# Performance work log

Hardware: AMD Instinct MI355X
Metric: run time of the kernel (lower is better)

The kernel has to match this reference:

```python
import jax, jax.numpy as jnp
import numpy as np

N = 10000        # nodes
E = 160000       # edges (avg degree 16)
MUL = 128        # channel multiplicity
A = 10           # node-attr (species one-hot) dim
RAD = 8          # radial bessel features
INV_SQRT3 = 0.5773502691896258  # CG coefficient for 1o x 1o -> 0e


def _mlp(x, Ws):
    # RadialMLP: linear layers with SiLU between, no activation on last
    for W in Ws[:-1]:
        x = jax.nn.silu(x @ W)
    return x @ Ws[-1]


def setup_inputs() -> dict:
    key = jax.random.key(0)
    ks = jax.random.split(key, 25)

    def g(k, shape):
        return jax.random.normal(k, shape, jnp.float32) / np.float32(np.sqrt(shape[0]))

    return {
        "node_attrs": jax.random.uniform(ks[0], (N, A), jnp.float32),
        "node_feats": jax.random.normal(ks[1], (N, 4 * MUL), jnp.float32),
        "edge_attrs": jax.random.normal(ks[2], (E, 4), jnp.float32),
        "edge_feats": jax.random.uniform(ks[3], (E, RAD), jnp.float32),
        "W_src": g(ks[5], (A, MUL)),
        "W_tgt": g(ks[6], (A, MUL)),
        "W_up0": g(ks[7], (MUL, MUL)),
        "W_up1": g(ks[8], (MUL, MUL)),
        "W_skip0": g(ks[9], (MUL, MUL)),
        "W_skip1": g(ks[10], (MUL, MUL)),
        "W_res0": g(ks[11], (MUL, 2 * MUL)),
        "W_res1": g(ks[12], (MUL, MUL)),
        "W_lin1_0": g(ks[13], (2 * MUL, 2 * MUL)),
        "W_lin1_1": g(ks[14], (2 * MUL, MUL)),
        "W_lin2_0": g(ks[15], (MUL, MUL)),
        "W_lin2_1": g(ks[16], (MUL, MUL)),
        "W_rad1": g(ks[17], (RAD + 2 * MUL, 64)),
        "W_rad2": g(ks[18], (64, 64)),
        "W_rad3": g(ks[19], (64, 64)),
        "W_rad4": g(ks[20], (64, 4 * MUL)),
        "W_den1": g(ks[21], (RAD + 2 * MUL, 64)),
        "W_den2": g(ks[22], (64, 1)),
        "alpha": jnp.ones((), jnp.float32),   # scaled by 20 inside (alpha = param * 20)
        "beta": jnp.zeros((), jnp.float32),
        "edge_index": jax.random.randint(ks[4], (E, 2), 0, N),
    }


def _forward(node_attrs, node_feats, edge_attrs, edge_feats,
             W_src, W_tgt, W_up0, W_up1, W_skip0, W_skip1, W_res0, W_res1,
             W_lin1_0, W_lin1_1, W_lin2_0, W_lin2_1,
             W_rad1, W_rad2, W_rad3, W_rad4, W_den1, W_den2,
             alpha, beta, edge_index):
    n = node_feats.shape[0]
    # split node feats into 128x0e scalars and 128x1o vectors (mul_ir layout)
    s = node_feats[:, :MUL]                           # [N, 128]
    v = node_feats[:, MUL:].reshape(n, MUL, 3)        # [N, 128, 3]

    # skip connection: Linear(node_feats_irreps -> hidden_irreps)
    sc_s = s @ W_skip0
    sc_v = jnp.einsum("nui,uv->nvi", v, W_skip1)
    sc = jnp.concatenate([sc_s, sc_v.reshape(n, -1)], axis=-1)  # [N, 512]

    # linear_up (node_feats -> edge_irreps) and linear_res (-> irreps_nonlin)
    up_s = s @ W_up0
    up_v = jnp.einsum("nui,uv->nvi", v, W_up1)
    res_s = s @ W_res0                                # [N, 256] (scalars + gates)
    res_v = jnp.einsum("nui,uv->nvi", v, W_res1)      # [N, 128, 3]

    # per-species scalar embeddings, gathered per edge
    src_emb = node_attrs @ W_src                      # [N, 128]
    tgt_emb = node_attrs @ W_tgt
    snd = edge_index[:, 0]
    rcv = edge_index[:, 1]
    aug = jnp.concatenate([edge_feats, src_emb[snd], tgt_emb[rcv]], axis=-1)  # [E, 264]

    # radial MLP -> per-edge tensor-product weights; density MLP
    tpw = _mlp(aug, [W_rad1, W_rad2, W_rad3, W_rad4])  # [E, 512]
    edge_density = jnp.tanh(_mlp(aug, [W_den1, W_den2]) ** 2)  # [E, 1]
    density = jax.ops.segment_sum(edge_density, rcv, num_segments=n)  # [N, 1]

    # equivariant tensor product (uvu, per-edge weights), lmax=1 CG paths
    xs = up_s[snd]                                    # [E, 128]
    xv = up_v[snd]                                    # [E, 128, 3]
    y0 = edge_attrs[:, :1]                            # [E, 1]
    y1 = edge_attrs[:, 1:4]                           # [E, 3]
    wA, wB, wC, wD = jnp.split(tpw, 4, axis=-1)
    mA = wA * xs * y0                                               # 0e x 0e -> 0e
    mD = wD * jnp.einsum("eui,ei->eu", xv, y1) * INV_SQRT3          # 1o x 1o -> 0e
    mB = (wB * xs)[:, :, None] * y1[:, None, :]                     # 0e x 1o -> 1o
    mC = wC[:, :, None] * xv * y0[:, :, None]                       # 1o x 0e -> 1o
    m_s = jnp.concatenate([mA, mD], axis=-1)          # [E, 256]
    m_v = jnp.concatenate([mB, mC], axis=1)           # [E, 256, 3]

    # scatter-add messages to receiver nodes
    msg_s = jax.ops.segment_sum(m_s, rcv, num_segments=n)  # [N, 256]
    msg_v = jax.ops.segment_sum(m_v, rcv, num_segments=n)  # [N, 256, 3]

    # linear_1 (irreps_mid -> irreps_nonlin), density normalization, residual
    msg_s = msg_s @ W_lin1_0                          # [N, 256]
    msg_v = jnp.einsum("nui,uv->nvi", msg_v, W_lin1_1)  # [N, 128, 3]
    denom = density * beta + alpha * 20.0             # [N, 1]
    msg_s = msg_s / denom + res_s
    msg_v = msg_v / denom[..., None] + res_v

    # equivariant gate nonlinearity: silu on scalars, sigmoid gates on vectors
    scal = jax.nn.silu(msg_s[:, :MUL])
    gate = jax.nn.sigmoid(msg_s[:, MUL:])
    vec = msg_v * gate[:, :, None]

    # linear_2 and reshape to [N, channels, (lmax+1)^2]
    out_s = scal @ W_lin2_0                           # [N, 128]
    out_v = jnp.einsum("nui,uv->nvi", vec, W_lin2_1)  # [N, 128, 3]
    message = jnp.concatenate([out_s[:, :, None], out_v], axis=-1)  # [N, 128, 4]
    return message, sc


def reference(node_attrs, node_feats, edge_attrs, edge_feats,
              W_src, W_tgt, W_up0, W_up1, W_skip0, W_skip1, W_res0, W_res1,
              W_lin1_0, W_lin1_1, W_lin2_0, W_lin2_1,
              W_rad1, W_rad2, W_rad3, W_rad4, W_den1, W_den2,
              alpha, beta, edge_index):
    return _forward(node_attrs, node_feats, edge_attrs, edge_feats,
                    W_src, W_tgt, W_up0, W_up1, W_skip0, W_skip1, W_res0, W_res1,
                    W_lin1_0, W_lin1_1, W_lin2_0, W_lin2_1,
                    W_rad1, W_rad2, W_rad3, W_rad4, W_den1, W_den2,
                    alpha, beta, edge_index)
```

## Files before the change

kernel.cpp:

```cpp
#include <hip/hip_runtime.h>
#include <hip/hip_bf16.h>
#include <math.h>

#define NN 10000
#define NE 160000
#define MUL 128
#define ADIM 10
#define RADF 8
#define HID 64
#define INV_SQRT3 0.57735026918962576f
#define NB64 157

typedef __attribute__((ext_vector_type(8))) short bf16x8;
typedef __attribute__((ext_vector_type(4))) float f32x4;

__device__ __forceinline__ float silu_f(float x){ return x / (1.0f + __expf(-x)); }
__device__ __forceinline__ float sigmoid_f(float x){ return 1.0f / (1.0f + __expf(-x)); }
__device__ __forceinline__ unsigned short f2b(float f){
  union{float f; unsigned u;} v; v.f=f;
  unsigned r = (v.u + 0x7fffu + ((v.u>>16)&1u))>>16;
  return (unsigned short)r;
}
__device__ __forceinline__ unsigned short f2bh(float f){
  __hip_bfloat16 h = __float2bfloat16(f);
  union{ __hip_bfloat16 h; unsigned short u; } v; v.h=h; return v.u;
}
__device__ __forceinline__ unsigned f2b2(float lo, float hi){
  float2 t; t.x=lo; t.y=hi;
  __hip_bfloat162 h2 = __float22bfloat162_rn(t);
  union{ __hip_bfloat162 h; unsigned u; } v; v.h=h2; return v.u;
}
__device__ __forceinline__ float b2f(unsigned short h){
  union{unsigned u; float f;} v; v.u = ((unsigned)h)<<16; return v.f;
}
__device__ __forceinline__ float b2f_lo(unsigned u){
  union{unsigned u; float f;} v; v.u = u<<16; return v.f;
}
__device__ __forceinline__ float b2f_hi(unsigned u){
  union{unsigned u; float f;} v; v.u = u & 0xffff0000u; return v.f;
}

__global__ __launch_bounds__(256) void k_nodeemb(
    const float* __restrict__ attrs, const float* __restrict__ Wc,
    float* __restrict__ pA, float* __restrict__ pB){
  int idx = blockIdx.x*256 + threadIdx.x;
  if (idx >= NN*64) return;
  int n = idx>>6, c = idx&63;
  float s0=0,s1=0,s2=0,s3=0;
  #pragma unroll
  for (int a=0;a<ADIM;a++){
    float x = attrs[n*ADIM+a];
    s0 += x*Wc[(0*ADIM+a)*64+c];
    s1 += x*Wc[(1*ADIM+a)*64+c];
    s2 += x*Wc[(2*ADIM+a)*64+c];
    s3 += x*Wc[(3*ADIM+a)*64+c];
  }
  pA[(size_t)n*128 + c*2 + 0] = s0;
  pA[(size_t)n*128 + c*2 + 1] = s2;
  pB[(size_t)n*128 + c*2 + 0] = s1;
  pB[(size_t)n*128 + c*2 + 1] = s3;
}

__global__ __launch_bounds__(256) void k_feat_prep(
    const float* __restrict__ feats, unsigned short* __restrict__ fs16,
    unsigned short* __restrict__ fv16){
  int idx = blockIdx.x*256 + threadIdx.x;
  int n = idx >> 9, c = idx & 511;
  float v = feats[idx];
  if (c < 128) fs16[n*128 + c] = f2bh(v);
  else {
    int q = c - 128; int u = q/3; int i = q - 3*u;
    fv16[((size_t)n*3 + i)*128 + u] = f2bh(v);
  }
}

__global__ __launch_bounds__(256) void k_prep(
    const float* __restrict__ Wr2, const float* __restrict__ Wr3,
    const float* __restrict__ Wr4,
    const float* __restrict__ Wl10, const float* __restrict__ Wl11,
    const float* __restrict__ Wl20, const float* __restrict__ Wl21,
    const float* __restrict__ Wsk0, const float* __restrict__ Wup0, const float* __restrict__ Wres0,
    const float* __restrict__ Wsk1, const float* __restrict__ Wup1, const float* __restrict__ Wres1,
    const float* __restrict__ Wsrc, const float* __restrict__ Wtgt,
    const float* __restrict__ Wr1, const float* __restrict__ Wd1,
    unsigned short* __restrict__ WTr2, unsigned short* __restrict__ WTr3,
    unsigned short* __restrict__ WTr4,
    unsigned short* __restrict__ Wl10T, unsigned short* __restrict__ Wl11T,
    unsigned short* __restrict__ Wl20T, unsigned short* __restrict__ Wl21T,
    unsigned short* __restrict__ WnsT, unsigned short* __restrict__ WnvT,
    float* __restrict__ Wc){
  int idx = blockIdx.x*256 + threadIdx.x;
  if (idx < 4096){
    int j = idx; int n=j>>6, k=j&63;
    WTr2[j] = f2b(Wr2[k*64+n]);
  } else if (idx < 8192){
    int j = idx-4096; int n=j>>6, k=j&63;
    WTr3[j] = f2b(Wr3[k*64+n]);
  } else if (idx < 40960){
    int j = idx-8192; int n=j>>6, k=j&63;
    WTr4[j] = f2b(Wr4[k*512+n]);
  } else if (idx < 106496){
    int j = idx-40960; int n=j>>8, k=j&255;
    Wl10T[j] = f2b(Wl10[k*256+n]);
  } else if (idx < 139264){
    int j = idx-106496; int n=j>>8, k=j&255;
    Wl11T[j] = f2b(Wl11[k*128+n]);
  } else if (idx < 155648){
    int j = idx-139264; int n=j>>7, k=j&127;
    Wl20T[j] = f2b(Wl20[k*128+n]);
  } else if (idx < 172032){
    int j = idx-155648; int n=j>>7, k=j&127;
    Wl21T[j] = f2b(Wl21[k*128+n]);
  } else if (idx < 237568){
    int j = idx-172032; int n=j>>7, k=j&127;
    float v;
    if (n < 128)      v = Wsk0[k*128+n];
    else if (n < 256) v = Wup0[k*128+(n-128)];
    else              v = Wres0[k*256+(n-256)];
    WnsT[j] = f2b(v);
  } else if (idx < 286720){
    int j = idx-237568; int n=j>>7, k=j&127;
    float v;
    if (n < 128)      v = Wsk1[k*128+n];
    else if (n < 256) v = Wup1[k*128+(n-128)];
    else              v = Wres1[k*128+(n-256)];
    WnvT[j] = f2b(v);
  } else if (idx < 286976){
    int j = idx - 286720;
    int m = j>>6, c = j&63;
    const float* WA = (m&1)? Wtgt : Wsrc;
    const float* WB = (m<2)? Wr1 : Wd1;
    int koff = (m&1)? 136 : 8;
    for (int a=0;a<ADIM;a++){
      float s=0.f;
      for (int k=0;k<128;k++) s += WA[a*128+k]*WB[(koff+k)*64+c];
      Wc[(m*ADIM+a)*64+c] = s;
    }
  }
}

__global__ __launch_bounds__(256) void k_node_pre2(
    const unsigned short* __restrict__ fs16, const unsigned short* __restrict__ fv16,
    const unsigned short* __restrict__ WnsT, const unsigned short* __restrict__ WnvT,
    float* __restrict__ out_sc,
    unsigned short* __restrict__ upk16,
    float* __restrict__ res_s, float* __restrict__ res_v){
  __shared__ unsigned short fA[64][136];
  int nb = blockIdx.x*64;
  int c = blockIdx.y;
  int g, ntc;
  if (c < 4){ g=0; ntc=c; } else { g = 1 + (c-4)/3; ntc = (c-4)%3; }
  int tid = threadIdx.x;
  int w = tid>>6, l = tid&63, m0 = w*16, lr = l&15, lg = l>>4;
  for (int idx=tid; idx<64*16; idx+=256){
    int row = idx>>4, s8 = idx&15;
    int n = min(nb+row, NN-1);
    const unsigned short* src = (g==0) ? &fs16[(size_t)n*128 + s8*8]
                                       : &fv16[((size_t)n*3 + (g-1))*128 + s8*8];
    *(uint4*)&fA[row][s8*8] = *(const uint4*)src;
  }
  __syncthreads();
  const unsigned short* WT = ((g==0)? WnsT : WnvT) + (size_t)ntc*128*128;
  f32x4 acc[8];
  #pragma unroll
  for (int t=0;t<8;t++) acc[t]=(f32x4)(0.f);
  #pragma unroll
  for (int kb=0;kb<4;kb++){
    bf16x8 a = *(const bf16x8*)&fA[m0+lr][kb*32 + lg*8];
    #pragma unroll
    for (int t=0;t<8;t++){
      bf16x8 b = *(const bf16x8*)&WT[(size_t)(t*16+lr)*128 + kb*32 + lg*8];
      acc[t] = __builtin_amdgcn_mfma_f32_16x16x32_bf16(a, b, acc[t], 0,0,0);
    }
  }
  #pragma unroll
  for (int t=0;t<8;t++){
    #pragma unroll
    for (int r=0;r<4;r++){
      int col = (ntc*8+t)*16 + lr;
      int row = m0 + lg*4 + r;
      int n = nb + row;
      if (n < NN){
        float v = acc[t][r];
        if (g==0){
          if (col < 128)      out_sc[(size_t)n*512 + col] = v;
          else if (col < 256){
            int cc = col-128;
            upk16[(size_t)n*512 + (cc&63)*8 + (cc>>6)] = f2bh(v);
          } else              res_s[(size_t)n*256 + col-256] = v;
        } else {
          int i = g-1;
          if (col < 128)      out_sc[(size_t)n*512 + 128 + col*3 + i] = v;
          else if (col < 256){
            int cc = col-128;
            upk16[(size_t)n*512 + (cc&63)*8 + (1+i)*2 + (cc>>6)] = f2bh(v);
          } else              res_v[((size_t)n*3+i)*128 + col-256] = v;
        }
      }
    }
  }
}

__global__ __launch_bounds__(256) void k_deg(const int* __restrict__ eidx, int* __restrict__ deg){
  int i = blockIdx.x*256+threadIdx.x;
  if (i<NE) atomicAdd(&deg[eidx[2*i+1]],1);
}
__global__ __launch_bounds__(256) void k_scan(const int* __restrict__ deg, int* __restrict__ offsets){
  __shared__ int part[256];
  int t = threadIdx.x; int base = t*40;
  int s=0;
  for (int k=0;k<40;k++){ int idx=base+k; if (idx<NN) s+=deg[idx]; }
  part[t]=s; __syncthreads();
  if (t==0){ int run=0; for (int i=0;i<256;i++){ int v=part[i]; part[i]=run; run+=v; } }
  __syncthreads();
  int run = part[t];
  for (int k=0;k<40;k++){
    int idx=base+k;
    if (idx<=NN) offsets[idx]=run;
    if (idx<NN) run+=deg[idx];
  }
}
__global__ __launch_bounds__(256) void k_fill(
    const int* __restrict__ eidx, const float* __restrict__ ef, const float* __restrict__ ea,
    const int* __restrict__ offsets, int* __restrict__ cursor,
    int* __restrict__ sndbuf, int* __restrict__ rcvbuf,
    float4* __restrict__ ybuf, float* __restrict__ efb){
  int i = blockIdx.x*256+threadIdx.x;
  if (i<NE){
    int sn = eidx[2*i], rc = eidx[2*i+1];
    int p = offsets[rc] + atomicAdd(&cursor[rc],1);
    sndbuf[p]=sn; rcvbuf[p]=rc;
    ybuf[p] = ((const float4*)ea)[i];
    *(float4*)&efb[(size_t)p*8]     = *(const float4*)&ef[(size_t)i*8];
    *(float4*)&efb[(size_t)p*8 + 4] = *(const float4*)&ef[(size_t)i*8 + 4];
  }
}

__global__ __launch_bounds__(256) void k_tpw(
    const int* __restrict__ sndbuf, const int* __restrict__ rcvbuf,
    const float* __restrict__ efb,
    const float* __restrict__ pA, const float* __restrict__ pB,
    const float* __restrict__ Wr1, const float* __restrict__ Wd1, const float* __restrict__ Wd2,
    const unsigned short* __restrict__ WTr2, const unsigned short* __restrict__ WTr3,
    const unsigned short* __restrict__ WTr4,
    const int* __restrict__ offsets, int nstart, int nend, int cap,
    unsigned* __restrict__ tpwp, float* __restrict__ densbuf){
  __shared__ unsigned short hA[64][72];
  __shared__ unsigned short hB[64][72];
  int ebase = offsets[nstart];
  int eend  = min(offsets[nend], ebase + cap);
  int i0 = ebase + blockIdx.x*64;
  if (i0 >= eend) return;
  int nrows = min(64, eend - i0);
  int tid = threadIdx.x;
  int w = tid>>6, l = tid&63, m0 = w*16, lr = l&15, lg = l>>4;
  int wbase = i0 + m0;
  int v_meta = 0;
  {
    int pos = min(wbase + (l&15), eend-1);
    if (l < 16)      v_meta = sndbuf[pos];
    else if (l < 32) v_meta = rcvbuf[pos];
  }
  float ra, rb;
  {
    int pos = min(wbase + (l&15), eend-1);
    ra = efb[(size_t)pos*8 + (l>>4)];
    rb = efb[(size_t)pos*8 + 4 + (l>>4)];
  }
  {
    float wr[8], wd[8];
    #pragma unroll
    for (int k=0;k<8;k++){ wr[k]=Wr1[k*64+l]; wd[k]=Wd1[k*64+l]; }
    float wd2c = Wd2[l];
    #pragma unroll
    for (int j=0;j<16;j++){
      int sn = __shfl(v_meta, j);
      int rc = __shfl(v_meta, 16+j);
      float2 av = *(const float2*)&pA[(size_t)sn*128 + l*2];
      float2 bv = *(const float2*)&pB[(size_t)rc*128 + l*2];
      float e0=__shfl(ra,j),    e1=__shfl(ra,16+j), e2=__shfl(ra,32+j), e3=__shfl(ra,48+j);
      float e4=__shfl(rb,j),    e5=__shfl(rb,16+j), e6=__shfl(rb,32+j), e7=__shfl(rb,48+j);
      float h  = av.x + bv.x;
      float hd = av.y + bv.y;
      h  += e0*wr[0]+e1*wr[1]+e2*wr[2]+e3*wr[3]+e4*wr[4]+e5*wr[5]+e6*wr[6]+e7*wr[7];
      hd += e0*wd[0]+e1*wd[1]+e2*wd[2]+e3*wd[3]+e4*wd[4]+e5*wd[5]+e6*wd[6]+e7*wd[7];
      hA[m0+j][l] = f2bh(silu_f(h));
      float sv = silu_f(hd)*wd2c;
      #pragma unroll
      for (int m=32;m;m>>=1) sv += __shfl_xor(sv, m);
      if (l==0 && m0+j < nrows) densbuf[wbase + j] = tanhf(sv*sv);
    }
  }
  f32x4 acc[4];
  #pragma unroll
  for (int nt=0;nt<4;nt++) acc[nt]=(f32x4)(0.f);
  #pragma unroll
  for (int kb=0;kb<2;kb++){
    bf16x8 a = *(const bf16x8*)&hA[m0+lr][kb*32 + lg*8];
    #pragma unroll
    for (int nt=0;nt<4;nt++){
      bf16x8 b = *(const bf16x8*)&WTr2[(nt*16+lr)*64 + kb*32 + lg*8];
      acc[nt] = __builtin_amdgcn_mfma_f32_16x16x32_bf16(a, b, acc[nt], 0,0,0);
    }
  }
  #pragma unroll
  for (int nt=0;nt<4;nt++)
    #pragma unroll
    for (int r=0;r<4;r++)
      hB[m0+lg*4+r][nt*16+lr] = f2bh(silu_f(acc[nt][r]));
  #pragma unroll
  for (int nt=0;nt<4;nt++) acc[nt]=(f32x4)(0.f);
  #pragma unroll
  for (int kb=0;kb<2;kb++){
    bf16x8 a = *(const bf16x8*)&hB[m0+lr][kb*32 + lg*8];
    #pragma unroll
    for (int nt=0;nt<4;nt++){
      bf16x8 b = *(const bf16x8*)&WTr3[(nt*16+lr)*64 + kb*32 + lg*8];
      acc[nt] = __builtin_amdgcn_mfma_f32_16x16x32_bf16(a, b, acc[nt], 0,0,0);
    }
  }
  #pragma unroll
  for (int nt=0;nt<4;nt++)
    #pragma unroll
    for (int r=0;r<4;r++)
      hA[m0+lg*4+r][nt*16+lr] = f2bh(silu_f(acc[nt][r]));
  int erow0 = i0 - ebase;
  #pragma unroll
  for (int nt=0; nt<4; nt++){
    unsigned pvv[4][4];
    #pragma unroll
    for (int G=0; G<4; G++){
      f32x4 aE=(f32x4)(0.f), aO=(f32x4)(0.f);
      #pragma unroll
      for (int kb=0; kb<2; kb++){
        bf16x8 a  = *(const bf16x8*)&hA[m0+lr][kb*32 + lg*8];
        bf16x8 bE = *(const bf16x8*)&WTr4[((2*G)*64+nt*16+lr)*64 + kb*32 + lg*8];
        bf16x8 bO = *(const bf16x8*)&WTr4[((2*G+1)*64+nt*16+lr)*64 + kb*32 + lg*8];
        aE = __builtin_amdgcn_mfma_f32_16x16x32_bf16(a, bE, aE, 0,0,0);
        aO = __builtin_amdgcn_mfma_f32_16x16x32_bf16(a, bO, aO, 0,0,0);
      }
      #pragma unroll
      for (int r=0;r<4;r++)
        pvv[r][G] = f2b2(aE[r], aO[r]);
    }
    #pragma unroll
    for (int r=0;r<4;r++){
      int row = m0 + lg*4 + r;
      if (row < nrows)
        *(uint4*)&tpwp[(size_t)(erow0+row)*256 + (nt*16+lr)*4] = *(uint4*)&pvv[r][0];
    }
  }
}

__global__ __launch_bounds__(256) void k_gather(
    const unsigned* __restrict__ tpwp, const float4* __restrict__ ybuf,
    const int* __restrict__ sndbuf, const float* __restrict__ densbuf,
    const uint4* __restrict__ upk4,
    const int* __restrict__ offsets, int nstart,
    unsigned short* __restrict__ msg_s16, unsigned short* __restrict__ msg_v16,
    float* __restrict__ density){
  __shared__ float part[2][1024];
  __shared__ float pden[2];
  int w = threadIdx.x>>6, l = threadIdx.x&63;
  int pairIdx = w>>1, half = w&1;
  int n = nstart + blockIdx.x*2 + pairIdx;
  int ebase = offsets[nstart];
  int s0 = offsets[n], s1 = offsets[n+1];
  float mA0=0,mA1=0,mD0=0,mD1=0;
  float mB00=0,mB01=0,mB10=0,mB11=0,mB20=0,mB21=0;
  float mC00=0,mC01=0,mC10=0,mC11=0,mC20=0,mC21=0;
  float dsum=0;
  for (int i=s0+half; i<s1; i+=2){
    int li = i - ebase;
    int sn = sndbuf[i];
    float4 y = ybuf[i];
    dsum += densbuf[i];
    uint4 tq = *(const uint4*)&tpwp[(size_t)li*256 + l*4];
    uint4 uq = upk4[(size_t)sn*64 + l];
    float wA0=b2f_lo(tq.x), wA1=b2f_hi(tq.x);
    float wB0=b2f_lo(tq.y), wB1=b2f_hi(tq.y);
    float wC0=b2f_lo(tq.z), wC1=b2f_hi(tq.z);
    float wD0=b2f_lo(tq.w), wD1=b2f_hi(tq.w);
    float xs0=b2f_lo(uq.x), xs1=b2f_hi(uq.x);
    float xv00=b2f_lo(uq.y), xv01=b2f_hi(uq.y);
    float xv10=b2f_lo(uq.z), xv11=b2f_hi(uq.z);
    float xv20=b2f_lo(uq.w), xv21=b2f_hi(uq.w);
    mA0 += wA0*xs0*y.x; mA1 += wA1*xs1*y.x;
    float dot0 = xv00*y.y + xv10*y.z + xv20*y.w;
    float dot1 = xv01*y.y + xv11*y.z + xv21*y.w;
    mD0 += wD0*dot0; mD1 += wD1*dot1;
    float b0 = wB0*xs0, b1 = wB1*xs1;
    mB00 += b0*y.y; mB01 += b1*y.y;
    mB10 += b0*y.z; mB11 += b1*y.z;
    mB20 += b0*y.w; mB21 += b1*y.w;
    float c0 = wC0*y.x, c1 = wC1*y.x;
    mC00 += c0*xv00; mC01 += c1*xv01;
    mC10 += c0*xv10; mC11 += c1*xv11;
    mC20 += c0*xv20; mC21 += c1*xv21;
  }
  if (half==1){
    float* P = part[pairIdx];
    P[0*64+l]=mA0;  P[1*64+l]=mA1;  P[2*64+l]=mD0;  P[3*64+l]=mD1;
    P[4*64+l]=mB00; P[5*64+l]=mB01; P[6*64+l]=mB10; P[7*64+l]=mB11;
    P[8*64+l]=mB20; P[9*64+l]=mB21; P[10*64+l]=mC00; P[11*64+l]=mC01;
    P[12*64+l]=mC10; P[13*64+l]=mC11; P[14*64+l]=mC20; P[15*64+l]=mC21;
    if (l==0) pden[pairIdx]=dsum;
  }
  __syncthreads();
  if (half==0){
    const float* P = part[pairIdx];
    mA0+=P[0*64+l];  mA1+=P[1*64+l];  mD0+=P[2*64+l];  mD1+=P[3*64+l];
    mB00+=P[4*64+l]; mB01+=P[5*64+l]; mB10+=P[6*64+l]; mB11+=P[7*64+l];
    mB20+=P[8*64+l]; mB21+=P[9*64+l]; mC00+=P[10*64+l]; mC01+=P[11*64+l];
    mC10+=P[12*64+l]; mC11+=P[13*64+l]; mC20+=P[14*64+l]; mC21+=P[15*64+l];
    dsum += pden[pairIdx];
    unsigned short* ms = msg_s16 + (size_t)n*256;
    ms[l]=f2bh(mA0); ms[64+l]=f2bh(mA1);
    ms[128+l]=f2bh(mD0*INV_SQRT3); ms[192+l]=f2bh(mD1*INV_SQRT3);
    unsigned short* mv = msg_v16 + (size_t)n*768;
    mv[l]=f2bh(mB00);     mv[64+l]=f2bh(mB01);  mv[128+l]=f2bh(mC00); mv[192+l]=f2bh(mC01);
    mv[256+l]=f2bh(mB10); mv[320+l]=f2bh(mB11); mv[384+l]=f2bh(mC10); mv[448+l]=f2bh(mC11);
    mv[512+l]=f2bh(mB20); mv[576+l]=f2bh(mB21); mv[640+l]=f2bh(mC20); mv[704+l]=f2bh(mC21);
    if (l==0) density[n]=dsum;
  }
}

__global__ __launch_bounds__(256) void k_post1(
    const unsigned short* __restrict__ msg_s16, const unsigned short* __restrict__ msg_v16,
    const float* __restrict__ density,
    const float* __restrict__ res_s, const float* __restrict__ res_v,
    const unsigned short* __restrict__ Wl10T, const unsigned short* __restrict__ Wl11T,
    const float* __restrict__ alphap, const float* __restrict__ betap,
    unsigned short* __restrict__ scal16, unsigned short* __restrict__ gate16,
    unsigned short* __restrict__ vtmp16){
  __shared__ unsigned short sm[64][264];
  __shared__ float sden[64];
  int nb = blockIdx.x*64, y = blockIdx.y;
  int tid = threadIdx.x;
  int w = tid>>6, l = tid&63, m0 = w*16, lr = l&15, lg = l>>4;
  for (int idx=tid; idx<64*32; idx+=256){
    int row = idx>>5, s8 = idx&31;
    int n = min(nb+row, NN-1);
    const unsigned short* src = (y<2)? &msg_s16[(size_t)n*256 + s8*8]
                                     : &msg_v16[(size_t)n*768 + (y-2)*256 + s8*8];
    *(uint4*)&sm[row][s8*8] = *(const uint4*)src;
  }
  if (tid < 64){
    int n = min(nb+tid, NN-1);
    sden[tid] = density[n]*betap[0] + alphap[0]*20.0f;
  }
  __syncthreads();
  const unsigned short* BT = (y<2)? (Wl10T + (size_t)y*128*256) : Wl11T;
  f32x4 acc[8];
  #pragma unroll
  for (int t=0;t<8;t++) acc[t]=(f32x4)(0.f);
  for (int kb=0;kb<8;kb++){
    bf16x8 a = *(const bf16x8*)&sm[m0+lr][kb*32 + lg*8];
    #pragma unroll
    for (int t=0;t<8;t++){
      bf16x8 b = *(const bf16x8*)&BT[(size_t)(t*16+lr)*256 + kb*32 + lg*8];
      acc[t] = __builtin_amdgcn_mfma_f32_16x16x32_bf16(a, b, acc[t], 0,0,0);
    }
  }
  #pragma unroll
  for (int t=0;t<8;t++){
    #pragma unroll
    for (int r=0;r<4;r++){
      int col = t*16+lr;
      int row = m0 + lg*4 + r;
      int n = nb + row;
      if (n < NN){
        float v = acc[t][r]/sden[row];
        if (y==0){
          v += res_s[(size_t)n*256 + col];
          scal16[(size_t)n*128 + col] = f2bh(silu_f(v));
        } else if (y==1){
          v += res_s[(size_t)n*256 + 128 + col];
          gate16[(size_t)n*128 + col] = f2bh(sigmoid_f(v));
        } else {
          int i = y-2;
          v += res_v[((size_t)n*3+i)*128 + col];
          vtmp16[((size_t)i*NN + n)*128 + col] = f2bh(v);
        }
      }
    }
  }
}

__global__ __launch_bounds__(256) void k_post2(
    const unsigned short* __restrict__ scal16, const unsigned short* __restrict__ gate16,
    const unsigned short* __restrict__ vtmp16,
    const unsigned short* __restrict__ Wl20T, const unsigned short* __restrict__ Wl21T,
    float* __restrict__ out_msg){
  __shared__ unsigned short sA[64][136];
  int nb = blockIdx.x*64, y = blockIdx.y;
  int tid = threadIdx.x;
  int w = tid>>6, l = tid&63, m0 = w*16, lr = l&15, lg = l>>4;
  for (int idx=tid; idx<64*16; idx+=256){
    int row = idx>>4, s8 = idx&15;
    int n = min(nb+row, NN-1);
    if (y==0){
      *(uint4*)&sA[row][s8*8] = *(const uint4*)&scal16[(size_t)n*128 + s8*8];
    } else {
      int i = y-1;
      uint4 va = *(const uint4*)&vtmp16[((size_t)i*NN + n)*128 + s8*8];
      uint4 vg = *(const uint4*)&gate16[(size_t)n*128 + s8*8];
      const unsigned short* pa = (const unsigned short*)&va;
      const unsigned short* pg = (const unsigned short*)&vg;
      unsigned short o[8];
      #pragma unroll
      for (int j=0;j<8;j++) o[j] = f2bh(b2f(pa[j])*b2f(pg[j]));
      *(uint4*)&sA[row][s8*8] = *(const uint4*)o;
    }
  }
  __syncthreads();
  const unsigned short* BT = (y==0)? Wl20T : Wl21T;
  f32x4 acc[8];
  #pragma unroll
  for (int t=0;t<8;t++) acc[t]=(f32x4)(0.f);
  #pragma unroll
  for (int kb=0;kb<4;kb++){
    bf16x8 a = *(const bf16x8*)&sA[m0+lr][kb*32 + lg*8];
    #pragma unroll
    for (int t=0;t<8;t++){
      bf16x8 b = *(const bf16x8*)&BT[(size_t)(t*16+lr)*128 + kb*32 + lg*8];
      acc[t] = __builtin_amdgcn_mfma_f32_16x16x32_bf16(a, b, acc[t], 0,0,0);
    }
  }
  #pragma unroll
  for (int t=0;t<8;t++){
    #pragma unroll
    for (int r=0;r<4;r++){
      int col = t*16+lr;
      int n = nb + m0 + lg*4 + r;
      if (n < NN) out_msg[(size_t)n*512 + col*4 + y] = acc[t][r];
    }
  }
}

extern "C" void kernel_launch(void* const* d_in, const int* in_sizes, int n_in,
                              void* d_out, int out_size, void* d_ws, size_t ws_size,
                              hipStream_t stream){
  (void)in_sizes; (void)n_in; (void)out_size;
  const float* attrs = (const float*)d_in[0];
  const float* feats = (const float*)d_in[1];
  const float* ea    = (const float*)d_in[2];
  const float* ef    = (const float*)d_in[3];
  const float* Wsrc  = (const float*)d_in[4];
  const float* Wtgt  = (const float*)d_in[5];
  const float* Wup0  = (const float*)d_in[6];
  const float* Wup1  = (const float*)d_in[7];
  const float* Wsk0  = (const float*)d_in[8];
  const float* Wsk1  = (const float*)d_in[9];
  const float* Wres0 = (const float*)d_in[10];
  const float* Wres1 = (const float*)d_in[11];
  const float* Wl10  = (const float*)d_in[12];
  const float* Wl11  = (const float*)d_in[13];
  const float* Wl20  = (const float*)d_in[14];
  const float* Wl21  = (const float*)d_in[15];
  const float* Wr1   = (const float*)d_in[16];
  const float* Wr2   = (const float*)d_in[17];
  const float* Wr3   = (const float*)d_in[18];
  const float* Wr4   = (const float*)d_in[19];
  const float* Wd1   = (const float*)d_in[20];
  const float* Wd2   = (const float*)d_in[21];
  const float* alphap= (const float*)d_in[22];
  const float* betap = (const float*)d_in[23];
  const int*   eidx  = (const int*)d_in[24];

  const size_t fixed_bytes =
      (size_t)NN*(512 + 1536 + 1024 + 1536 + 4 + 1024 + 256 + 768 + 512 + 512 + 256) +
      (size_t)NE*60 +
      (size_t)286976*2 + 4*ADIM*64*4 +
      (10240+10240+10256)*4 + 64*256;
  int nchunk, npc, cap;
  if (fixed_bytes + (size_t)NE*1024 + 65536 <= ws_size){ nchunk=1; npc=NN;   cap=NE;    }
  else if (fixed_bytes + 81920ULL*1024 + 65536 <= ws_size){ nchunk=2; npc=5000; cap=81920; }
  else { nchunk=4; npc=2500; cap=44032; }

  char* p = (char*)d_ws;
  auto alloc = [&](size_t bytes)->char*{ char* r=p; p += (bytes+255)&~(size_t)255; return r; };
  unsigned* tpwp  = (unsigned*)alloc((size_t)cap*256*4);
  unsigned short* msg_s16 = (unsigned short*)alloc((size_t)NN*256*2);
  unsigned short* msg_v16 = (unsigned short*)alloc((size_t)NN*768*2);
  float*  res_s   = (float*)alloc((size_t)NN*256*4);
  float*  res_v   = (float*)alloc((size_t)NN*384*4);
  float*  density = (float*)alloc((size_t)NN*4);
  float4* ybuf    = (float4*)alloc((size_t)NE*16);
  float*  densbuf = (float*)alloc((size_t)NE*4);
  int*    sndbuf  = (int*)alloc((size_t)NE*4);
  int*    rcvbuf  = (int*)alloc((size_t)NE*4);
  float*  efb     = (float*)alloc((size_t)NE*32);
  uint4*  upk     = (uint4*)alloc((size_t)NN*64*16);
  unsigned short* fs16 = (unsigned short*)alloc((size_t)NN*128*2);
  unsigned short* fv16 = (unsigned short*)alloc((size_t)NN*384*2);
  float* pA = (float*)alloc((size_t)NN*128*4);
  float* pB = (float*)alloc((size_t)NN*128*4);
  float* Wc  = (float*)alloc(4*ADIM*64*4);
  unsigned short* gate16 = (unsigned short*)alloc((size_t)NN*128*2);
  unsigned short* WTr2 = (unsigned short*)alloc(4096*2);
  unsigned short* WTr3 = (unsigned short*)alloc(4096*2);
  unsigned short* WTr4 = (unsigned short*)alloc(32768*2);
  unsigned short* Wl10T = (unsigned short*)alloc(65536*2);
  unsigned short* Wl11T = (unsigned short*)alloc(32768*2);
  unsigned short* Wl20T = (unsigned short*)alloc(16384*2);
  unsigned short* Wl21T = (unsigned short*)alloc(16384*2);
  unsigned short* WnsT  = (unsigned short*)alloc(65536*2);
  unsigned short* WnvT  = (unsigned short*)alloc(49152*2);
  int* deg     = (int*)alloc(10240*4);
  int* cursor  = (int*)alloc(10240*4);
  int* offsets = (int*)alloc(10256*4);

  unsigned short* scal16 = fs16;
  unsigned short* vtmp16 = fv16;

  float* out_msg = (float*)d_out;
  float* out_sc  = out_msg + (size_t)NN*512;

  hipMemsetAsync(deg, 0, 2*10240*sizeof(int), stream);

  k_prep<<<1121, 256, 0, stream>>>(Wr2, Wr3, Wr4, Wl10, Wl11, Wl20, Wl21,
                                   Wsk0, Wup0, Wres0, Wsk1, Wup1, Wres1,
                                   Wsrc, Wtgt, Wr1, Wd1,
                                   WTr2, WTr3, WTr4,
                                   Wl10T, Wl11T, Wl20T, Wl21T, WnsT, WnvT, Wc);
  k_nodeemb<<<(NN*64+255)/256, 256, 0, stream>>>(attrs, Wc, pA, pB);
  k_feat_prep<<<NN*512/256, 256, 0, stream>>>(feats, fs16, fv16);
  k_node_pre2<<<dim3(NB64,13), 256, 0, stream>>>(fs16, fv16, WnsT, WnvT,
                                                 out_sc, (unsigned short*)upk, res_s, res_v);
  k_deg<<<(NE+255)/256, 256, 0, stream>>>(eidx, deg);
  k_scan<<<1, 256, 0, stream>>>(deg, offsets);
  k_fill<<<(NE+255)/256, 256, 0, stream>>>(eidx, ef, ea, offsets, cursor,
                                           sndbuf, rcvbuf, ybuf, efb);

  int tpw_blocks = (cap+63)/64;
  for (int c=0; c<nchunk; ++c){
    k_tpw<<<tpw_blocks, 256, 0, stream>>>(sndbuf, rcvbuf, efb, pA, pB,
                                          Wr1, Wd1, Wd2, WTr2, WTr3, WTr4,
                                          offsets, c*npc, (c+1)*npc, cap,
                                          tpwp, densbuf);
    k_gather<<<npc/2, 256, 0, stream>>>(tpwp, ybuf, sndbuf, densbuf, upk,
                                        offsets, c*npc, msg_s16, msg_v16, density);
  }

  k_post1<<<dim3(NB64,5), 256, 0, stream>>>(msg_s16, msg_v16, density, res_s, res_v,
                                            Wl10T, Wl11T, alphap, betap,
                                            scal16, gate16, vtmp16);
  k_post2<<<dim3(NB64,4), 256, 0, stream>>>(scal16, gate16, vtmp16,
                                            Wl20T, Wl21T, out_msg);
}
```

Before: 442.9 us.

## Fuse edge MLP with receiver segmented reduction, add boundary fixup kernel

Merges the per-edge radial MLP kernel and the per-node gather kernel into one. Each wave takes a fixed 16-edge window, reduces it by receiver segment in registers, and writes interior segments straight to fp32 message buffers. Segments that cross a window boundary go to head/tail partial buffers, which a new fixup kernel combines. This removes the large bf16 per-edge weight buffer, its write and re-read, and the chunk loop. The cost is extra fp32 message traffic, a memset of the message buffers, and scattered boundary writes.

```diff
diff --git a/kernel.cpp b/kernel.cpp
--- a/kernel.cpp
+++ b/kernel.cpp
@@ -10,6 +10,8 @@
 #define HID 64
 #define INV_SQRT3 0.57735026918962576f
 #define NB64 157
+#define WEDGE 16
+#define NWIN (NE/WEDGE)
 
 typedef __attribute__((ext_vector_type(8))) short bf16x8;
 typedef __attribute__((ext_vector_type(4))) float f32x4;
@@ -236,42 +238,38 @@
   }
 }
 
-__global__ __launch_bounds__(256) void k_tpw(
+__global__ __launch_bounds__(256) void k_edge(
     const int* __restrict__ sndbuf, const int* __restrict__ rcvbuf,
-    const float* __restrict__ efb,
+    const float* __restrict__ efb, const float4* __restrict__ ybuf,
     const float* __restrict__ pA, const float* __restrict__ pB,
     const float* __restrict__ Wr1, const float* __restrict__ Wd1, const float* __restrict__ Wd2,
     const unsigned short* __restrict__ WTr2, const unsigned short* __restrict__ WTr3,
     const unsigned short* __restrict__ WTr4,
-    const int* __restrict__ offsets, int nstart, int nend, int cap,
-    unsigned* __restrict__ tpwp, float* __restrict__ densbuf){
+    const int* __restrict__ offsets, const uint4* __restrict__ upk4,
+    float* __restrict__ msg_s, float* __restrict__ msg_v, float* __restrict__ density,
+    float* __restrict__ pbufH, float* __restrict__ pbufT,
+    float* __restrict__ pbufHd, float* __restrict__ pbufTd){
   __shared__ unsigned short hA[64][72];
   __shared__ unsigned short hB[64][72];
-  int ebase = offsets[nstart];
-  int eend  = min(offsets[nend], ebase + cap);
-  int i0 = ebase + blockIdx.x*64;
-  if (i0 >= eend) return;
-  int nrows = min(64, eend - i0);
+  __shared__ unsigned pv[4][16][132];
+  __shared__ float sy[64][4];
   int tid = threadIdx.x;
   int w = tid>>6, l = tid&63, m0 = w*16, lr = l&15, lg = l>>4;
-  int wbase = i0 + m0;
+  int W = blockIdx.x*4 + w;
+  int wbase = W*WEDGE;
+  int pos = wbase + (l&15);
   int v_meta = 0;
-  {
-    int pos = min(wbase + (l&15), eend-1);
-    if (l < 16)      v_meta = sndbuf[pos];
-    else if (l < 32) v_meta = rcvbuf[pos];
-  }
-  float ra, rb;
-  {
-    int pos = min(wbase + (l&15), eend-1);
-    ra = efb[(size_t)pos*8 + (l>>4)];
-    rb = efb[(size_t)pos*8 + 4 + (l>>4)];
-  }
+  if (l < 16)      v_meta = sndbuf[pos];
+  else if (l < 32) v_meta = rcvbuf[pos];
+  float ra = efb[(size_t)pos*8 + (l>>4)];
+  float rb = efb[(size_t)pos*8 + 4 + (l>>4)];
+  if (l < 16) *(float4*)&sy[m0+l][0] = ybuf[wbase + l];
   {
     float wr[8], wd[8];
     #pragma unroll
     for (int k=0;k<8;k++){ wr[k]=Wr1[k*64+l]; wd[k]=Wd1[k*64+l]; }
     float wd2c = Wd2[l];
+    float dAcc = 0.f;
     #pragma unroll
     for (int j=0;j<16;j++){
       int sn = __shfl(v_meta, j);
@@ -288,145 +286,174 @@
       float sv = silu_f(hd)*wd2c;
       #pragma unroll
       for (int m=32;m;m>>=1) sv += __shfl_xor(sv, m);
-      if (l==0 && m0+j < nrows) densbuf[wbase + j] = tanhf(sv*sv);
-    }
-  }
-  f32x4 acc[4];
-  #pragma unroll
-  for (int nt=0;nt<4;nt++) acc[nt]=(f32x4)(0.f);
-  #pragma unroll
-  for (int kb=0;kb<2;kb++){
-    bf16x8 a = *(const bf16x8*)&hA[m0+lr][kb*32 + lg*8];
-    #pragma unroll
-    for (int nt=0;nt<4;nt++){
-      bf16x8 b = *(const bf16x8*)&WTr2[(nt*16+lr)*64 + kb*32 + lg*8];
-      acc[nt] = __builtin_amdgcn_mfma_f32_16x16x32_bf16(a, b, acc[nt], 0,0,0);
-    }
-  }
-  #pragma unroll
-  for (int nt=0;nt<4;nt++)
-    #pragma unroll
-    for (int r=0;r<4;r++)
-      hB[m0+lg*4+r][nt*16+lr] = f2bh(silu_f(acc[nt][r]));
-  #pragma unroll
-  for (int nt=0;nt<4;nt++) acc[nt]=(f32x4)(0.f);
-  #pragma unroll
-  for (int kb=0;kb<2;kb++){
-    bf16x8 a = *(const bf16x8*)&hB[m0+lr][kb*32 + lg*8];
-    #pragma unroll
-    for (int nt=0;nt<4;nt++){
-      bf16x8 b = *(const bf16x8*)&WTr3[(nt*16+lr)*64 + kb*32 + lg*8];
-      acc[nt] = __builtin_amdgcn_mfma_f32_16x16x32_bf16(a, b, acc[nt], 0,0,0);
-    }
-  }
-  #pragma unroll
-  for (int nt=0;nt<4;nt++)
-    #pragma unroll
-    for (int r=0;r<4;r++)
-      hA[m0+lg*4+r][nt*16+lr] = f2bh(silu_f(acc[nt][r]));
-  int erow0 = i0 - ebase;
-  #pragma unroll
-  for (int nt=0; nt<4; nt++){
-    unsigned pvv[4][4];
-    #pragma unroll
-    for (int G=0; G<4; G++){
-      f32x4 aE=(f32x4)(0.f), aO=(f32x4)(0.f);
+      dAcc += 1.f - 2.f/(1.f + __expf(2.f*sv*sv));
+      int rcn = (j<15)? __shfl(v_meta, 16+j+1) : -1;
+      if (j==15 || rc != rcn){
+        if (l==0){
+          bool head = offsets[rc] < wbase;
+          bool tail = offsets[rc+1] > wbase+WEDGE;
+          if (head) pbufHd[W]=dAcc;
+          if (tail) pbufTd[W]=dAcc;
+          if (!head && !tail) density[rc]=dAcc;
+        }
+        dAcc=0.f;
+      }
+    }
+  }
+  {
+    f32x4 acc[4];
+    #pragma unroll
+    for (int nt=0;nt<4;nt++) acc[nt]=(f32x4)(0.f);
+    #pragma unroll
+    for (int kb=0;kb<2;kb++){
+      bf16x8 a = *(const bf16x8*)&hA[m0+lr][kb*32 + lg*8];
       #pragma unroll
-      for (int kb=0; kb<2; kb++){
-        bf16x8 a  = *(const bf16x8*)&hA[m0+lr][kb*32 + lg*8];
-        bf16x8 bE = *(const bf16x8*)&WTr4[((2*G)*64+nt*16+lr)*64 + kb*32 + lg*8];
-        bf16x8 bO = *(const bf16x8*)&WTr4[((2*G+1)*64+nt*16+lr)*64 + kb*32 + lg*8];
-        aE = __builtin_amdgcn_mfma_f32_16x16x32_bf16(a, bE, aE, 0,0,0);
-        aO = __builtin_amdgcn_mfma_f32_16x16x32_bf16(a, bO, aO, 0,0,0);
-      }
+      for (int nt=0;nt<4;nt++){
+        bf16x8 b = *(const bf16x8*)&WTr2[(nt*16+lr)*64 + kb*32 + lg*8];
+        acc[nt] = __builtin_amdgcn_mfma_f32_16x16x32_bf16(a, b, acc[nt], 0,0,0);
+      }
+    }
+    #pragma unroll
+    for (int nt=0;nt<4;nt++)
       #pragma unroll
       for (int r=0;r<4;r++)
-        pvv[r][G] = f2b2(aE[r], aO[r]);
-    }
-    #pragma unroll
-    for (int r=0;r<4;r++){
-      int row = m0 + lg*4 + r;
-      if (row < nrows)
-        *(uint4*)&tpwp[(size_t)(erow0+row)*256 + (nt*16+lr)*4] = *(uint4*)&pvv[r][0];
-    }
-  }
-}
-
-__global__ __launch_bounds__(256) void k_gather(
-    const unsigned* __restrict__ tpwp, const float4* __restrict__ ybuf,
-    const int* __restrict__ sndbuf, const float* __restrict__ densbuf,
-    const uint4* __restrict__ upk4,
-    const int* __restrict__ offsets, int nstart,
-    unsigned short* __restrict__ msg_s16, unsigned short* __restrict__ msg_v16,
-    float* __restrict__ density){
-  __shared__ float part[2][1024];
-  __shared__ float pden[2];
-  int w = threadIdx.x>>6, l = threadIdx.x&63;
-  int pairIdx = w>>1, half = w&1;
-  int n = nstart + blockIdx.x*2 + pairIdx;
-  int ebase = offsets[nstart];
+        hB[m0+lg*4+r][nt*16+lr] = f2bh(silu_f(acc[nt][r]));
+  }
+  {
+    f32x4 acc[4];
+    #pragma unroll
+    for (int nt=0;nt<4;nt++) acc[nt]=(f32x4)(0.f);
+    #pragma unroll
+    for (int kb=0;kb<2;kb++){
+      bf16x8 a = *(const bf16x8*)&hB[m0+lr][kb*32 + lg*8];
+      #pragma unroll
+      for (int nt=0;nt<4;nt++){
+        bf16x8 b = *(const bf16x8*)&WTr3[(nt*16+lr)*64 + kb*32 + lg*8];
+        acc[nt] = __builtin_amdgcn_mfma_f32_16x16x32_bf16(a, b, acc[nt], 0,0,0);
+      }
+    }
+    #pragma unroll
+    for (int nt=0;nt<4;nt++)
+      #pragma unroll
+      for (int r=0;r<4;r++)
+        hA[m0+lg*4+r][nt*16+lr] = f2bh(silu_f(acc[nt][r]));
+  }
+  #pragma unroll
+  for (int pass=0; pass<2; ++pass){
+    #pragma unroll
+    for (int gg=0; gg<2; ++gg){
+      int G = pass*2 + gg;
+      #pragma unroll
+      for (int nt=0; nt<4; nt++){
+        f32x4 aE=(f32x4)(0.f), aO=(f32x4)(0.f);
+        #pragma unroll
+        for (int kb=0; kb<2; kb++){
+          bf16x8 a  = *(const bf16x8*)&hA[m0+lr][kb*32 + lg*8];
+          bf16x8 bE = *(const bf16x8*)&WTr4[((2*G)*64+nt*16+lr)*64 + kb*32 + lg*8];
+          bf16x8 bO = *(const bf16x8*)&WTr4[((2*G+1)*64+nt*16+lr)*64 + kb*32 + lg*8];
+          aE = __builtin_amdgcn_mfma_f32_16x16x32_bf16(a, bE, aE, 0,0,0);
+          aO = __builtin_amdgcn_mfma_f32_16x16x32_bf16(a, bO, aO, 0,0,0);
+        }
+        #pragma unroll
+        for (int r=0;r<4;r++)
+          pv[w][lg*4+r][gg*66 + nt*16+lr] = f2b2(aE[r], aO[r]);
+      }
+    }
+    float a0=0,a1=0,b00=0,b01=0,b10=0,b11=0,b20=0,b21=0;
+    #pragma unroll
+    for (int j=0;j<16;j++){
+      int sn = __shfl(v_meta, j);
+      int rc = __shfl(v_meta, 16+j);
+      unsigned p0 = pv[w][j][l];
+      unsigned p1 = pv[w][j][66+l];
+      float4 y = *(const float4*)&sy[m0+j][0];
+      if (pass==0){
+        unsigned xs = ((const unsigned*)upk4)[((size_t)sn*64 + l)*4];
+        float xs0=b2f_lo(xs), xs1=b2f_hi(xs);
+        a0 += b2f_lo(p0)*xs0*y.x;  a1 += b2f_hi(p0)*xs1*y.x;
+        float t0 = b2f_lo(p1)*xs0, t1 = b2f_hi(p1)*xs1;
+        b00 += t0*y.y; b01 += t1*y.y;
+        b10 += t0*y.z; b11 += t1*y.z;
+        b20 += t0*y.w; b21 += t1*y.w;
+      } else {
+        uint4 uq = upk4[(size_t)sn*64 + l];
+        float xv00=b2f_lo(uq.y), xv01=b2f_hi(uq.y);
+        float xv10=b2f_lo(uq.z), xv11=b2f_hi(uq.z);
+        float xv20=b2f_lo(uq.w), xv21=b2f_hi(uq.w);
+        float c0 = b2f_lo(p0)*y.x, c1 = b2f_hi(p0)*y.x;
+        b00 += c0*xv00; b01 += c1*xv01;
+        b10 += c0*xv10; b11 += c1*xv11;
+        b20 += c0*xv20; b21 += c1*xv21;
+        float dot0 = xv00*y.y + xv10*y.z + xv20*y.w;
+        float dot1 = xv01*y.y + xv11*y.z + xv21*y.w;
+        a0 += b2f_lo(p1)*dot0; a1 += b2f_hi(p1)*dot1;
+      }
+      int rcn = (j<15)? __shfl(v_meta, 16+j+1) : -1;
+      if (j==15 || rc != rcn){
+        bool head = offsets[rc] < wbase;
+        bool tail = offsets[rc+1] > wbase+WEDGE;
+        float sA0, sA1;
+        if (pass==0){ sA0=a0; sA1=a1; }
+        else        { sA0=a0*INV_SQRT3; sA1=a1*INV_SQRT3; }
+        int soff = (pass==0)? 0 : 128;
+        int voff = (pass==0)? 0 : 128;
+        if (head){
+          float* pb = pbufH + (size_t)W*1024;
+          pb[soff+l]=sA0; pb[soff+64+l]=sA1;
+          float* qb = pb + 256;
+          qb[voff+l]=b00; qb[voff+64+l]=b01;
+          qb[voff+256+l]=b10; qb[voff+320+l]=b11;
+          qb[voff+512+l]=b20; qb[voff+576+l]=b21;
+        }
+        if (tail){
+          float* pb = pbufT + (size_t)W*1024;
+          pb[soff+l]=sA0; pb[soff+64+l]=sA1;
+          float* qb = pb + 256;
+          qb[voff+l]=b00; qb[voff+64+l]=b01;
+          qb[voff+256+l]=b10; qb[voff+320+l]=b11;
+          qb[voff+512+l]=b20; qb[voff+576+l]=b21;
+        }
+        if (!head && !tail){
+          float* ps = msg_s + (size_t)rc*256;
+          ps[soff+l]=sA0; ps[soff+64+l]=sA1;
+          float* pvv = msg_v + (size_t)rc*768;
+          pvv[voff+l]=b00; pvv[voff+64+l]=b01;
+          pvv[voff+256+l]=b10; pvv[voff+320+l]=b11;
+          pvv[voff+512+l]=b20; pvv[voff+576+l]=b21;
+        }
+        a0=0;a1=0;b00=0;b01=0;b10=0;b11=0;b20=0;b21=0;
+      }
+    }
+  }
+}
+
+__global__ __launch_bounds__(256) void k_fixup(
+    const int* __restrict__ offsets,
+    const float* __restrict__ pbufH, const float* __restrict__ pbufT,
+    const float* __restrict__ pbufHd, const float* __restrict__ pbufTd,
+    float* __restrict__ msg_s, float* __restrict__ msg_v, float* __restrict__ density){
+  int n = blockIdx.x*4 + (threadIdx.x>>6);
+  if (n >= NN) return;
+  int l = threadIdx.x & 63;
   int s0 = offsets[n], s1 = offsets[n+1];
-  float mA0=0,mA1=0,mD0=0,mD1=0;
-  float mB00=0,mB01=0,mB10=0,mB11=0,mB20=0,mB21=0;
-  float mC00=0,mC01=0,mC10=0,mC11=0,mC20=0,mC21=0;
-  float dsum=0;
-  for (int i=s0+half; i<s1; i+=2){
-    int li = i - ebase;
-    int sn = sndbuf[i];
-    float4 y = ybuf[i];
-    dsum += densbuf[i];
-    uint4 tq = *(const uint4*)&tpwp[(size_t)li*256 + l*4];
-    uint4 uq = upk4[(size_t)sn*64 + l];
-    float wA0=b2f_lo(tq.x), wA1=b2f_hi(tq.x);
-    float wB0=b2f_lo(tq.y), wB1=b2f_hi(tq.y);
-    float wC0=b2f_lo(tq.z), wC1=b2f_hi(tq.z);
-    float wD0=b2f_lo(tq.w), wD1=b2f_hi(tq.w);
-    float xs0=b2f_lo(uq.x), xs1=b2f_hi(uq.x);
-    float xv00=b2f_lo(uq.y), xv01=b2f_hi(uq.y);
-    float xv10=b2f_lo(uq.z), xv11=b2f_hi(uq.z);
-    float xv20=b2f_lo(uq.w), xv21=b2f_hi(uq.w);
-    mA0 += wA0*xs0*y.x; mA1 += wA1*xs1*y.x;
-    float dot0 = xv00*y.y + xv10*y.z + xv20*y.w;
-    float dot1 = xv01*y.y + xv11*y.z + xv21*y.w;
-    mD0 += wD0*dot0; mD1 += wD1*dot1;
-    float b0 = wB0*xs0, b1 = wB1*xs1;
-    mB00 += b0*y.y; mB01 += b1*y.y;
-    mB10 += b0*y.z; mB11 += b1*y.z;
-    mB20 += b0*y.w; mB21 += b1*y.w;
-    float c0 = wC0*y.x, c1 = wC1*y.x;
-    mC00 += c0*xv00; mC01 += c1*xv01;
-    mC10 += c0*xv10; mC11 += c1*xv11;
-    mC20 += c0*xv20; mC21 += c1*xv21;
-  }
-  if (half==1){
-    float* P = part[pairIdx];
-    P[0*64+l]=mA0;  P[1*64+l]=mA1;  P[2*64+l]=mD0;  P[3*64+l]=mD1;
-    P[4*64+l]=mB00; P[5*64+l]=mB01; P[6*64+l]=mB10; P[7*64+l]=mB11;
-    P[8*64+l]=mB20; P[9*64+l]=mB21; P[10*64+l]=mC00; P[11*64+l]=mC01;
-    P[12*64+l]=mC10; P[13*64+l]=mC11; P[14*64+l]=mC20; P[15*64+l]=mC21;
-    if (l==0) pden[pairIdx]=dsum;
-  }
-  __syncthreads();
-  if (half==0){
-    const float* P = part[pairIdx];
-    mA0+=P[0*64+l];  mA1+=P[1*64+l];  mD0+=P[2*64+l];  mD1+=P[3*64+l];
-    mB00+=P[4*64+l]; mB01+=P[5*64+l]; mB10+=P[6*64+l]; mB11+=P[7*64+l];
-    mB20+=P[8*64+l]; mB21+=P[9*64+l]; mC00+=P[10*64+l]; mC01+=P[11*64+l];
-    mC10+=P[12*64+l]; mC11+=P[13*64+l]; mC20+=P[14*64+l]; mC21+=P[15*64+l];
-    dsum += pden[pairIdx];
-    unsigned short* ms = msg_s16 + (size_t)n*256;
-    ms[l]=f2bh(mA0); ms[64+l]=f2bh(mA1);
-    ms[128+l]=f2bh(mD0*INV_SQRT3); ms[192+l]=f2bh(mD1*INV_SQRT3);
-    unsigned short* mv = msg_v16 + (size_t)n*768;
-    mv[l]=f2bh(mB00);     mv[64+l]=f2bh(mB01);  mv[128+l]=f2bh(mC00); mv[192+l]=f2bh(mC01);
-    mv[256+l]=f2bh(mB10); mv[320+l]=f2bh(mB11); mv[384+l]=f2bh(mC10); mv[448+l]=f2bh(mC11);
-    mv[512+l]=f2bh(mB20); mv[576+l]=f2bh(mB21); mv[640+l]=f2bh(mC20); mv[704+l]=f2bh(mC21);
-    if (l==0) density[n]=dsum;
+  if (s1 <= s0) return;
+  int a = s0/WEDGE, b = (s1-1)/WEDGE;
+  if (a == b) return;
+  for (int c=l; c<1024; c+=64){
+    float v = pbufT[(size_t)a*1024 + c];
+    for (int m=a+1; m<=b; ++m) v += pbufH[(size_t)m*1024 + c];
+    if (c < 256) msg_s[(size_t)n*256 + c] = v;
+    else         msg_v[(size_t)n*768 + (c-256)] = v;
+  }
+  if (l==0){
+    float dv = pbufTd[a];
+    for (int m=a+1; m<=b; ++m) dv += pbufHd[m];
+    density[n] = dv;
   }
 }
 
 __global__ __launch_bounds__(256) void k_post1(
-    const unsigned short* __restrict__ msg_s16, const unsigned short* __restrict__ msg_v16,
+    const float* __restrict__ msg_s, const float* __restrict__ msg_v,
     const float* __restrict__ density,
     const float* __restrict__ res_s, const float* __restrict__ res_v,
     const unsigned short* __restrict__ Wl10T, const unsigned short* __restrict__ Wl11T,
@@ -441,9 +468,11 @@
   for (int idx=tid; idx<64*32; idx+=256){
     int row = idx>>5, s8 = idx&31;
     int n = min(nb+row, NN-1);
-    const unsigned short* src = (y<2)? &msg_s16[(size_t)n*256 + s8*8]
-                                     : &msg_v16[(size_t)n*768 + (y-2)*256 + s8*8];
-    *(uint4*)&sm[row][s8*8] = *(const uint4*)src;
+    const float* src = (y<2)? &msg_s[(size_t)n*256 + s8*8]
+                            : &msg_v[(size_t)n*768 + (y-2)*256 + s8*8];
+    float4 a0 = *(const float4*)src, a1 = *(const float4*)(src+4);
+    unsigned o4[4] = { f2b2(a0.x,a0.y), f2b2(a0.z,a0.w), f2b2(a1.x,a1.y), f2b2(a1.z,a1.w) };
+    *(uint4*)&sm[row][s8*8] = *(uint4*)o4;
   }
   if (tid < 64){
     int n = min(nb+tid, NN-1);
@@ -541,7 +570,7 @@
 extern "C" void kernel_launch(void* const* d_in, const int* in_sizes, int n_in,
                               void* d_out, int out_size, void* d_ws, size_t ws_size,
                               hipStream_t stream){
-  (void)in_sizes; (void)n_in; (void)out_size;
+  (void)in_sizes; (void)n_in; (void)out_size; (void)ws_size;
   const float* attrs = (const float*)d_in[0];
   const float* feats = (const float*)d_in[1];
   const float* ea    = (const float*)d_in[2];
@@ -568,26 +597,18 @@
   const float* betap = (const float*)d_in[23];
   const int*   eidx  = (const int*)d_in[24];
 
-  const size_t fixed_bytes =
-      (size_t)NN*(512 + 1536 + 1024 + 1536 + 4 + 1024 + 256 + 768 + 512 + 512 + 256) +
-      (size_t)NE*60 +
-      (size_t)286976*2 + 4*ADIM*64*4 +
-      (10240+10240+10256)*4 + 64*256;
-  int nchunk, npc, cap;
-  if (fixed_bytes + (size_t)NE*1024 + 65536 <= ws_size){ nchunk=1; npc=NN;   cap=NE;    }
-  else if (fixed_bytes + 81920ULL*1024 + 65536 <= ws_size){ nchunk=2; npc=5000; cap=81920; }
-  else { nchunk=4; npc=2500; cap=44032; }
-
   char* p = (char*)d_ws;
   auto alloc = [&](size_t bytes)->char*{ char* r=p; p += (bytes+255)&~(size_t)255; return r; };
-  unsigned* tpwp  = (unsigned*)alloc((size_t)cap*256*4);
-  unsigned short* msg_s16 = (unsigned short*)alloc((size_t)NN*256*2);
-  unsigned short* msg_v16 = (unsigned short*)alloc((size_t)NN*768*2);
+  float*  msg_s32 = (float*)alloc((size_t)NN*256*4);
+  float*  msg_v32 = (float*)alloc((size_t)NN*768*4);
+  float*  density = (float*)alloc((size_t)NN*4);
+  float*  pbufH   = (float*)alloc((size_t)NWIN*1024*4);
+  float*  pbufT   = (float*)alloc((size_t)NWIN*1024*4);
+  float*  pbufHd  = (float*)alloc((size_t)NWIN*4);
+  float*  pbufTd  = (float*)alloc((size_t)NWIN*4);
   float*  res_s   = (float*)alloc((size_t)NN*256*4);
   float*  res_v   = (float*)alloc((size_t)NN*384*4);
-  float*  density = (float*)alloc((size_t)NN*4);
   float4* ybuf    = (float4*)alloc((size_t)NE*16);
-  float*  densbuf = (float*)alloc((size_t)NE*4);
   int*    sndbuf  = (int*)alloc((size_t)NE*4);
   int*    rcvbuf  = (int*)alloc((size_t)NE*4);
   float*  efb     = (float*)alloc((size_t)NE*32);
@@ -617,6 +638,7 @@
   float* out_msg = (float*)d_out;
   float* out_sc  = out_msg + (size_t)NN*512;
 
+  hipMemsetAsync(msg_s32, 0, (size_t)NN*(256+768+1)*4, stream);
   hipMemsetAsync(deg, 0, 2*10240*sizeof(int), stream);
 
   k_prep<<<1121, 256, 0, stream>>>(Wr2, Wr3, Wr4, Wl10, Wl11, Wl20, Wl21,
@@ -633,17 +655,15 @@
   k_fill<<<(NE+255)/256, 256, 0, stream>>>(eidx, ef, ea, offsets, cursor,
                                            sndbuf, rcvbuf, ybuf, efb);
 
-  int tpw_blocks = (cap+63)/64;
-  for (int c=0; c<nchunk; ++c){
-    k_tpw<<<tpw_blocks, 256, 0, stream>>>(sndbuf, rcvbuf, efb, pA, pB,
-                                          Wr1, Wd1, Wd2, WTr2, WTr3, WTr4,
-                                          offsets, c*npc, (c+1)*npc, cap,
-                                          tpwp, densbuf);
-    k_gather<<<npc/2, 256, 0, stream>>>(tpwp, ybuf, sndbuf, densbuf, upk,
-                                        offsets, c*npc, msg_s16, msg_v16, density);
-  }
-
-  k_post1<<<dim3(NB64,5), 256, 0, stream>>>(msg_s16, msg_v16, density, res_s, res_v,
+  k_edge<<<NE/64, 256, 0, stream>>>(sndbuf, rcvbuf, efb, ybuf, pA, pB,
+                                    Wr1, Wd1, Wd2, WTr2, WTr3, WTr4,
+                                    offsets, upk,
+                                    msg_s32, msg_v32, density,
+                                    pbufH, pbufT, pbufHd, pbufTd);
+  k_fixup<<<(NN+3)/4, 256, 0, stream>>>(offsets, pbufH, pbufT, pbufHd, pbufTd,
+                                        msg_s32, msg_v32, density);
+
+  k_post1<<<dim3(NB64,5), 256, 0, stream>>>(msg_s32, msg_v32, density, res_s, res_v,
                                             Wl10T, Wl11T, alphap, betap,
                                             scal16, gate16, vtmp16);
   k_post2<<<dim3(NB64,4), 256, 0, stream>>>(scal16, gate16, vtmp16,
```

Measured after the change: 466.1 us. 1.05x slower.
